# Kernel optimization log

Measured on AMD Instinct MI355X. Metric: run time of the kernel, lower is better.

## Reference

```python
import jax, jax.numpy as jnp
import numpy as np

N, E, C = 100000, 50000, 256
M, D, F, T = 128, 128, 128, 64
MSG = 2 * D + F + T  # 448
T_MAX = 100000


def setup_inputs() -> dict:
    key = jax.random.key(0)
    ks = jax.random.split(key, 16)
    src = jax.random.randint(ks[0], (E,), 0, N, dtype=jnp.int32)
    dst = jax.random.randint(ks[1], (E,), 0, N, dtype=jnp.int32)
    t = jnp.sort(jax.random.randint(ks[2], (E,), 0, T_MAX, dtype=jnp.int32))
    last_update = jax.random.randint(ks[3], (N,), 0, 1000, dtype=jnp.int32)
    event_feat = jax.random.normal(ks[4], (E, F), dtype=jnp.float32)
    src_embeds = jax.random.normal(ks[5], (E, D), dtype=jnp.float32)
    dst_embeds = jax.random.normal(ks[6], (E, D), dtype=jnp.float32)
    nodes_memory = jax.random.normal(ks[7], (N, M), dtype=jnp.float32)
    incidence = jax.random.uniform(ks[8], (N, C), dtype=jnp.float32)
    w_time = jax.random.normal(ks[9], (T,), dtype=jnp.float32)
    b_time = jax.random.normal(ks[10], (T,), dtype=jnp.float32)
    W_ih = jax.random.normal(ks[11], (MSG, 3 * M), dtype=jnp.float32) * 0.05
    W_hh = jax.random.normal(ks[12], (M, 3 * M), dtype=jnp.float32) * 0.05
    b_ih = jnp.zeros((3 * M,), jnp.float32)
    b_hh = jnp.zeros((3 * M,), jnp.float32)
    return dict(src=src, dst=dst, t=t, last_update=last_update,
                event_feat=event_feat, src_embeds=src_embeds, dst_embeds=dst_embeds,
                nodes_memory=nodes_memory, incidence=incidence,
                w_time=w_time, b_time=b_time, W_ih=W_ih, W_hh=W_hh,
                b_ih=b_ih, b_hh=b_hh)


def reference(src, dst, t, last_update, event_feat, src_embeds, dst_embeds,
              nodes_memory, incidence, w_time, b_time, W_ih, W_hh, b_ih, b_hh):
    E2 = 2 * E
    # store_events: raw messages + flipped-direction messages, keyed by source node
    src_all = jnp.concatenate([src, dst])            # [2E]
    emb_s = jnp.concatenate([src_embeds, dst_embeds], axis=0)
    emb_d = jnp.concatenate([dst_embeds, src_embeds], axis=0)
    feat = jnp.concatenate([event_feat, event_feat], axis=0)
    t_all = jnp.concatenate([t, t])                  # [2E]
    # message function: concat(src_embed, dst_embed, event_feat, time_encoding(dt))
    dt = (t_all - last_update[src_all]).astype(jnp.float32)
    time_enc = jnp.cos(dt[:, None] * w_time[None, :] + b_time[None, :])  # [2E, T]
    msg = jnp.concatenate([emb_s, emb_d, feat, time_enc], axis=-1)       # [2E, MSG]
    # 'last' aggregation: per-node argmax over timestamps via rank-encoded segment_max
    perm = jnp.argsort(t_all)  # ascending time order
    rank = jnp.zeros((E2,), jnp.int32).at[perm].set(jnp.arange(E2, dtype=jnp.int32))
    seg_rank = jax.ops.segment_max(rank, src_all, num_segments=N)
    counts = jax.ops.segment_sum(jnp.ones((E2,), jnp.int32), src_all, num_segments=N)
    has_msg = counts > 0                              # [N]
    last_idx = perm[jnp.where(has_msg, seg_rank, 0)]  # [N] event index of last message
    agg_msg = msg[last_idx]                           # [N, MSG]
    # GRU memory updater (torch.nn.GRUCell convention)
    gx = agg_msg @ W_ih + b_ih
    gh = nodes_memory @ W_hh + b_hh
    xr, xz, xn = jnp.split(gx, 3, axis=-1)
    hr, hz, hn = jnp.split(gh, 3, axis=-1)
    r = jax.nn.sigmoid(xr + hr)
    z = jax.nn.sigmoid(xz + hz)
    n = jnp.tanh(xn + r * hn)
    h_new = (1.0 - z) * n + z * nodes_memory
    new_mem = jnp.where(has_msg[:, None], h_new, nodes_memory)  # [N, M]
    # rewire_graph: community memory = incidence.T @ nodes_memory
    comm_mem = jnp.einsum('nc,nm->cm', incidence, new_mem)      # [C, M]
    return jnp.concatenate([new_mem, comm_mem], axis=0)         # [N + C, M]
```

## Files before the change

### kernel.cpp

```cpp
#include <hip/hip_runtime.h>
#include <hip/hip_bf16.h>
#include <stdint.h>

#define N_NODES   100000
#define N_EVENTS  50000
#define N_COMM    256
#define DIM_M     128
#define K_TOT     576
#define GCOLS     512
#define INV2PI    0.15915494309189535f
#define XB_GRID   4096
#define WCONV_BLOCKS ((GCOLS * K_TOT + 255) / 256)
#define COPY_BLOCKS  512

typedef float f32x4 __attribute__((ext_vector_type(4)));
typedef short s16x8 __attribute__((ext_vector_type(8)));
typedef short s16x4 __attribute__((ext_vector_type(4)));

#define KEYS_OFF   0
#define CNT_OFF    800000
#define LIST_OFF   800008
#define WT_OFF     1200640
#define X_ROWS     100096
#define X_OFF      1790464
#define PART_M_OFF X_OFF
#define CT_NCH     512
#define CT_CPN     196
#define TMP2_OFF   (PART_M_OFF + 67108864)
#define TENC_OFF   1790464
#define PART_F_OFF 14594560

__device__ inline unsigned short f2bf(float x) {
    union { float f; unsigned u; } v; v.f = x;
    unsigned r = v.u + 0x7FFFu + ((v.u >> 16) & 1u);
    return (unsigned short)(r >> 16);
}
__device__ inline float bf2f(unsigned short u) {
    union { unsigned u; float f; } v; v.u = ((unsigned)u) << 16;
    return v.f;
}
__device__ inline float cos_rev(float rev) {
    float fr = rev - floorf(rev);
#if __has_builtin(__builtin_amdgcn_cosf)
    return __builtin_amdgcn_cosf(fr);
#else
    return cosf(fr * 6.283185307179586f);
#endif
}
__device__ inline float sigmoid_f(float x) { return 1.0f / (1.0f + __expf(-x)); }
__device__ inline float tanh_f(float x) {
    float t = __expf(2.0f * x);
    return 1.0f - 2.0f / (t + 1.0f);
}

__global__ __launch_bounds__(256) void k_agg(const int* __restrict__ src,
                                             const int* __restrict__ dst,
                                             const int* __restrict__ t,
                                             unsigned long long* __restrict__ keys) {
    int i = blockIdx.x * 256 + threadIdx.x;
    if (i >= 2 * N_EVENTS) return;
    int e = (i < N_EVENTS) ? i : i - N_EVENTS;
    int node = (i < N_EVENTS) ? src[i] : dst[e];
    unsigned long long key =
        ((unsigned long long)(unsigned)t[e] << 32) | (unsigned)(i + 1);
    atomicMax(&keys[node], key);
}

__global__ __launch_bounds__(256) void k_compact(const unsigned long long* __restrict__ keys,
                                                 unsigned int* __restrict__ cnt,
                                                 int* __restrict__ list) {
    int n = blockIdx.x * 256 + threadIdx.x;
    if (n >= N_NODES) return;
    if (keys[n] != 0ULL) {
        unsigned p = atomicAdd(cnt, 1u);
        list[p] = n;
    }
}

__global__ __launch_bounds__(256) void k_xbuild(
    const unsigned long long* __restrict__ keys,
    const unsigned int* __restrict__ cnt,
    const int* __restrict__ list,
    const int* __restrict__ t,
    const int* __restrict__ last_update,
    const float* __restrict__ event_feat,
    const float* __restrict__ src_embeds,
    const float* __restrict__ dst_embeds,
    const float* __restrict__ mem,
    const float* __restrict__ w_time,
    const float* __restrict__ b_time,
    const float* __restrict__ W_ih,
    const float* __restrict__ W_hh,
    unsigned short* __restrict__ Wt,
    unsigned short* __restrict__ X,
    float* __restrict__ out) {
    if (blockIdx.x >= XB_GRID + WCONV_BLOCKS) {
        const int b = blockIdx.x - (XB_GRID + WCONV_BLOCKS);
        for (int idx = b * 256 + threadIdx.x; idx < N_NODES * 32;
             idx += COPY_BLOCKS * 256) {
            const int n = idx >> 5;
            if (keys[n] == 0ULL)
                ((float4*)out)[idx] = ((const float4*)mem)[idx];
        }
        return;
    }
    if (blockIdx.x >= XB_GRID) {
        int idx = (blockIdx.x - XB_GRID) * 256 + threadIdx.x;
        if (idx >= GCOLS * K_TOT) return;
        int col2 = idx / K_TOT, k = idx % K_TOT;
        int mh = col2 >> 8, rem = col2 & 255;
        int g = rem >> 6, m = mh * 64 + (rem & 63);
        float v;
        if (g == 0)      v = (k < 448) ? W_ih[(size_t)k * 384 + m]
                                       : W_hh[(size_t)(k - 448) * 384 + m];
        else if (g == 1) v = (k < 448) ? W_ih[(size_t)k * 384 + 128 + m]
                                       : W_hh[(size_t)(k - 448) * 384 + 128 + m];
        else if (g == 2) v = (k < 448) ? W_ih[(size_t)k * 384 + 256 + m] : 0.0f;
        else             v = (k < 448) ? 0.0f : W_hh[(size_t)(k - 448) * 384 + 256 + m];
        Wt[idx] = f2bf(v);
        return;
    }
    const unsigned c = *cnt;
    const unsigned cpad = (c + 127u) & ~127u;
    const unsigned total = cpad * 72u;
    for (unsigned idx = blockIdx.x * 256 + threadIdx.x; idx < total;
         idx += XB_GRID * 256) {
        const unsigned row = idx / 72u;
        const int s = (int)(idx - row * 72u);
        unsigned short* xp = X + (size_t)row * K_TOT + s * 8;
        s16x8 v;
        if (row >= c) {
#pragma unroll
            for (int j = 0; j < 8; ++j) v[j] = 0;
            *(s16x8*)xp = v;
            continue;
        }
        const int node = list[row];
        const unsigned long long key = keys[node];
        const int ia = (int)(key & 0xffffffffull) - 1;
        const int e = (ia < N_EVENTS) ? ia : ia - N_EVENTS;
        if (s < 48) {
            const float* p;
            if (s < 16)
                p = ((ia < N_EVENTS) ? src_embeds : dst_embeds) + (size_t)e * 128 + s * 8;
            else if (s < 32)
                p = ((ia < N_EVENTS) ? dst_embeds : src_embeds) + (size_t)e * 128 + (s - 16) * 8;
            else
                p = event_feat + (size_t)e * 128 + (s - 32) * 8;
            float4 a = *(const float4*)p;
            float4 b = *(const float4*)(p + 4);
            v[0] = (short)f2bf(a.x); v[1] = (short)f2bf(a.y);
            v[2] = (short)f2bf(a.z); v[3] = (short)f2bf(a.w);
            v[4] = (short)f2bf(b.x); v[5] = (short)f2bf(b.y);
            v[6] = (short)f2bf(b.z); v[7] = (short)f2bf(b.w);
        } else if (s < 56) {
            const float dt = (float)(t[e] - last_update[node]);
            const int c0 = (s - 48) * 8;
#pragma unroll
            for (int j = 0; j < 8; ++j) {
                float rev = fmaf(dt, w_time[c0 + j] * INV2PI, b_time[c0 + j] * INV2PI);
                v[j] = (short)f2bf(cos_rev(rev));
            }
        } else {
            const float* p = mem + (size_t)node * 128 + (s - 56) * 8;
            float4 a = *(const float4*)p;
            float4 b = *(const float4*)(p + 4);
            v[0] = (short)f2bf(a.x); v[1] = (short)f2bf(a.y);
            v[2] = (short)f2bf(a.z); v[3] = (short)f2bf(a.w);
            v[4] = (short)f2bf(b.x); v[5] = (short)f2bf(b.y);
            v[6] = (short)f2bf(b.z); v[7] = (short)f2bf(b.w);
        }
        *(s16x8*)xp = v;
    }
}

__global__ __launch_bounds__(512, 4) void k_gemm2(
    const unsigned int* __restrict__ cnt,
    const int* __restrict__ list,
    const unsigned short* __restrict__ X,
    const unsigned short* __restrict__ Wt,
    const float* __restrict__ b_ih,
    const float* __restrict__ b_hh,
    float* __restrict__ out) {
    __shared__ unsigned short As[3][128][32];
    __shared__ unsigned short Bs[3][256][32];
    __shared__ int Ls[128];

    const unsigned c = *cnt;
    const int rb = blockIdx.x >> 1;
    const int mh = blockIdx.x & 1;
    const int base = rb * 128;
    if ((unsigned)base >= c) return;
    const int tid = threadIdx.x;
    const int w = tid >> 6, l = tid & 63;
    const int lr = l & 15, lk = l >> 4;
    const int wm = w >> 2, wn = w & 3;

    if (tid < 128)
        Ls[tid] = ((unsigned)(base + tid) < c) ? list[base + tid] : 0;

    const int mcol = mh * 64 + wn * 16 + lr;

    unsigned short hreg[16];
#pragma unroll
    for (int rt = 0; rt < 4; ++rt)
#pragma unroll
        for (int reg = 0; reg < 4; ++reg) {
            const int r = wm * 64 + rt * 16 + lk * 4 + reg;
            hreg[rt * 4 + reg] = X[(size_t)(base + r) * K_TOT + 448 + mcol];
        }

    const int srow = tid >> 2;
    const int sd = tid & 3;
    const int ssl = (sd ^ ((srow >> 1) & 3)) << 3;
    const unsigned short* gA  = X  + (size_t)(base + srow) * K_TOT + ssl;
    const unsigned short* gB0 = Wt + (size_t)(mh * 256 + srow) * K_TOT + ssl;
    const unsigned short* gB1 = Wt + (size_t)(mh * 256 + 128 + srow) * K_TOT + ssl;

#define GLD(SRC, DST) __builtin_amdgcn_global_load_lds( \
        (const __attribute__((address_space(1))) unsigned int*)(SRC), \
        (__attribute__((address_space(3))) unsigned int*)(DST), 16, 0, 0)

    auto stage = [&](int ch, int buf) {
        GLD(gA  + ch * 32, &As[buf][w * 16][0]);
        GLD(gB0 + ch * 32, &Bs[buf][w * 16][0]);
        GLD(gB1 + ch * 32, &Bs[buf][128 + w * 16][0]);
    };

    f32x4 acc[4][4];
#pragma unroll
    for (int rt = 0; rt < 4; ++rt)
#pragma unroll
        for (int i = 0; i < 4; ++i) acc[rt][i] = (f32x4){0.f, 0.f, 0.f, 0.f};

    stage(0, 0);
    stage(1, 1);
    __syncthreads();

#pragma unroll
    for (int ch = 0; ch < 18; ++ch) {
        const int buf = ch % 3;
        if (ch <= 15) stage(ch + 2, (ch + 2) % 3);
        __builtin_amdgcn_s_setprio(1);
        s16x8 a[4];
#pragma unroll
        for (int rt = 0; rt < 4; ++rt) {
            const int r = wm * 64 + rt * 16 + lr;
            const int sl = lk ^ ((r >> 1) & 3);
            a[rt] = *(const s16x8*)&As[buf][r][sl << 3];
        }
#pragma unroll
        for (int i = 0; i < 4; ++i) {
            const int cl = i * 64 + wn * 16 + lr;
            const int slb = lk ^ ((cl >> 1) & 3);
            s16x8 b = *(const s16x8*)&Bs[buf][cl][slb << 3];
#pragma unroll
            for (int rt = 0; rt < 4; ++rt)
                acc[rt][i] = __builtin_amdgcn_mfma_f32_16x16x32_bf16(
                    a[rt], b, acc[rt][i], 0, 0, 0);
        }
        __builtin_amdgcn_s_setprio(0);
        if (ch < 17) {
            __builtin_amdgcn_sched_barrier(0);
            if (ch < 16) asm volatile("s_waitcnt vmcnt(3)" ::: "memory");
            else         asm volatile("s_waitcnt vmcnt(0)" ::: "memory");
            __builtin_amdgcn_s_barrier();
            __builtin_amdgcn_sched_barrier(0);
        }
    }

    const float b_r  = b_ih[mcol] + b_hh[mcol];
    const float b_z  = b_ih[128 + mcol] + b_hh[128 + mcol];
    const float b_xn = b_ih[256 + mcol];
    const float b_hn = b_hh[256 + mcol];
#pragma unroll
    for (int rt = 0; rt < 4; ++rt) {
#pragma unroll
        for (int reg = 0; reg < 4; ++reg) {
            const int r = wm * 64 + rt * 16 + lk * 4 + reg;
            const int grow = base + r;
            if ((unsigned)grow < c) {
                const int node = Ls[r];
                const float h = bf2f(hreg[rt * 4 + reg]);
                float rr = sigmoid_f(acc[rt][0][reg] + b_r);
                float zz = sigmoid_f(acc[rt][1][reg] + b_z);
                float nn = tanh_f(acc[rt][2][reg] + b_xn + rr * (acc[rt][3][reg] + b_hn));
                out[(size_t)node * 128 + mcol] = (1.0f - zz) * nn + zz * h;
            }
        }
    }
#undef GLD
}

__global__ __launch_bounds__(256) void k_copy(const unsigned long long* __restrict__ keys,
                                              const float* __restrict__ nm,
                                              float* __restrict__ out) {
    int idx = blockIdx.x * 256 + threadIdx.x;
    int n = idx >> 5;
    if (n >= N_NODES) return;
    if (keys[n] != 0ULL) return;
    ((float4*)out)[idx] = ((const float4*)nm)[idx];
}

__global__ __launch_bounds__(512) void k_comm_t(const float* __restrict__ inc,
                                                const float* __restrict__ nm,
                                                float* __restrict__ partials) {
    __shared__ unsigned short T[2][12288];

    const int bid = blockIdx.x;
    const int n0 = bid * CT_CPN;
    const int n1 = min(N_NODES, n0 + CT_CPN);
    const int ng = (n1 - n0 + 31) >> 5;
    const int tid = threadIdx.x;
    const int w = tid >> 6, l = tid & 63;
    const int lr = l & 15, lk = l >> 4;

    float vi[4][4];
    float vm[4][2];

    auto load_chunk = [&](int g) {
        const int nb = n0 + g * 32 + w * 4;
#pragma unroll
        for (int ri = 0; ri < 4; ++ri) {
            const int n = nb + ri;
            const bool ok = n < n1;
#pragma unroll
            for (int j = 0; j < 4; ++j)
                vi[ri][j] = ok ? inc[(size_t)n * N_COMM + l + 64 * j] : 0.0f;
#pragma unroll
            for (int j = 0; j < 2; ++j)
                vm[ri][j] = ok ? nm[(size_t)n * DIM_M + l + 64 * j] : 0.0f;
        }
    };
    auto write_chunk = [&](int buf) {
        unsigned short* bi = &T[buf][0];
#pragma unroll
        for (int j = 0; j < 4; ++j) {
            const int cc = l + 64 * j;
            ushort4 p = make_ushort4(f2bf(vi[0][j]), f2bf(vi[1][j]),
                                     f2bf(vi[2][j]), f2bf(vi[3][j]));
            *(ushort4*)&bi[cc * 32 + ((w ^ (cc & 7)) << 2)] = p;
        }
        unsigned short* bm = &T[buf][8192];
#pragma unroll
        for (int j = 0; j < 2; ++j) {
            const int mm = l + 64 * j;
            ushort4 p = make_ushort4(f2bf(vm[0][j]), f2bf(vm[1][j]),
                                     f2bf(vm[2][j]), f2bf(vm[3][j]));
            *(ushort4*)&bm[mm * 32 + ((w ^ (mm & 7)) << 2)] = p;
        }
    };

    f32x4 acc[2][8];
#pragma unroll
    for (int ct = 0; ct < 2; ++ct)
#pragma unroll
        for (int mt = 0; mt < 8; ++mt) acc[ct][mt] = (f32x4){0.f, 0.f, 0.f, 0.f};

    auto compute_chunk = [&](int buf) {
        const unsigned short* bi = &T[buf][0];
        const unsigned short* bm = &T[buf][8192];
        s16x8 a[2];
#pragma unroll
        for (int ct = 0; ct < 2; ++ct) {
            const int cc = (w * 2 + ct) * 16 + lr;
            s16x4 lo = *(const s16x4*)&bi[cc * 32 + (((lk * 2) ^ (cc & 7)) << 2)];
            s16x4 hi = *(const s16x4*)&bi[cc * 32 + (((lk * 2 + 1) ^ (cc & 7)) << 2)];
            a[ct] = __builtin_shufflevector(lo, hi, 0, 1, 2, 3, 4, 5, 6, 7);
        }
#pragma unroll
        for (int mt = 0; mt < 8; ++mt) {
            const int mm = mt * 16 + lr;
            s16x4 lo = *(const s16x4*)&bm[mm * 32 + (((lk * 2) ^ (mm & 7)) << 2)];
            s16x4 hi = *(const s16x4*)&bm[mm * 32 + (((lk * 2 + 1) ^ (mm & 7)) << 2)];
            s16x8 b = __builtin_shufflevector(lo, hi, 0, 1, 2, 3, 4, 5, 6, 7);
            acc[0][mt] = __builtin_amdgcn_mfma_f32_16x16x32_bf16(a[0], b, acc[0][mt], 0, 0, 0);
            acc[1][mt] = __builtin_amdgcn_mfma_f32_16x16x32_bf16(a[1], b, acc[1][mt], 0, 0, 0);
        }
    };

    load_chunk(0);
    write_chunk(0);
    __syncthreads();
    for (int g = 0; g < ng; ++g) {
        if (g + 1 < ng) load_chunk(g + 1);
        compute_chunk(g & 1);
        if (g + 1 < ng) write_chunk((g + 1) & 1);
        __syncthreads();
    }

    float* p = partials + (size_t)bid * (N_COMM * DIM_M);
#pragma unroll
    for (int ct = 0; ct < 2; ++ct)
#pragma unroll
        for (int mt = 0; mt < 8; ++mt)
            *(f32x4*)&p[(size_t)(((ct * 8 + mt) * 512) + tid) * 4] = acc[ct][mt];
}

__global__ __launch_bounds__(256) void k_comm2a(const float* __restrict__ partials,
                                                float* __restrict__ tmp) {
    const int bid = blockIdx.x;
    const int y = bid >> 5, x = bid & 31;
    const int idx4 = x * 256 + threadIdx.x;
    float4 s = make_float4(0.f, 0.f, 0.f, 0.f);
    for (int ci = 0; ci < CT_NCH / 32; ++ci) {
        float4 v = *(const float4*)&partials[(size_t)(y * (CT_NCH / 32) + ci) * (N_COMM * DIM_M) + idx4 * 4];
        s.x += v.x; s.y += v.y; s.z += v.z; s.w += v.w;
    }
    *(float4*)&tmp[(size_t)y * (N_COMM * DIM_M) + idx4 * 4] = s;
}

__global__ __launch_bounds__(256) void k_comm2b(const float* __restrict__ tmp,
                                                float* __restrict__ out) {
    const int idx4 = blockIdx.x * 256 + threadIdx.x;
    float4 s = make_float4(0.f, 0.f, 0.f, 0.f);
    for (int y = 0; y < 32; ++y) {
        float4 v = *(const float4*)&tmp[(size_t)y * (N_COMM * DIM_M) + idx4 * 4];
        s.x += v.x; s.y += v.y; s.z += v.z; s.w += v.w;
    }
    const int q = idx4 >> 9;
    const int tid = idx4 & 511;
    const int ct = q >> 3, mt = q & 7;
    const int w = tid >> 6, l = tid & 63;
    const int lr = l & 15, lk = l >> 4;
    const int mm = mt * 16 + lr;
    const float sv[4] = {s.x, s.y, s.z, s.w};
#pragma unroll
    for (int reg = 0; reg < 4; ++reg) {
        const int cc = (w * 2 + ct) * 16 + lk * 4 + reg;
        out[(size_t)N_NODES * DIM_M + (size_t)cc * DIM_M + mm] = sv[reg];
    }
}

__global__ __launch_bounds__(256) void k_wconv_old(const float* __restrict__ W_ih,
                                                   const float* __restrict__ W_hh,
                                                   unsigned short* __restrict__ Wt) {
    int idx = blockIdx.x * 256 + threadIdx.x;
    if (idx >= GCOLS * K_TOT) return;
    int col = idx / K_TOT, k = idx % K_TOT;
    float v;
    if (col < 256) {
        v = (k < 448) ? W_ih[(size_t)k * 384 + col]
                      : W_hh[(size_t)(k - 448) * 384 + col];
    } else if (col < 384) {
        v = (k < 448) ? W_ih[(size_t)k * 384 + col] : 0.0f;
    } else {
        v = (k < 448) ? 0.0f : W_hh[(size_t)(k - 448) * 384 + (col - 128)];
    }
    Wt[idx] = f2bf(v);
}

__global__ __launch_bounds__(256) void k_tenc(const unsigned long long* __restrict__ keys,
                                              const unsigned int* __restrict__ cnt,
                                              const int* __restrict__ list,
                                              const int* __restrict__ t,
                                              const int* __restrict__ last_update,
                                              const float* __restrict__ w_time,
                                              const float* __restrict__ b_time,
                                              unsigned short* __restrict__ tenc) {
    int idx = blockIdx.x * 256 + threadIdx.x;
    int r = idx >> 3, slot = idx & 7;
    const unsigned c = *cnt;
    const unsigned cpad = (c + 63u) & ~63u;
    if ((unsigned)r >= cpad) return;
    s16x8 v;
    if ((unsigned)r < c) {
        int node = list[r];
        unsigned long long key = keys[node];
        int ia = (int)(key & 0xffffffffull) - 1;
        int e = (ia < N_EVENTS) ? ia : ia - N_EVENTS;
        float dt = (float)(t[e] - last_update[node]);
#pragma unroll
        for (int j = 0; j < 8; ++j) {
            int cix = slot * 8 + j;
            float arg = __fadd_rn(__fmul_rn(dt, w_time[cix]), b_time[cix]);
            v[j] = (short)f2bf(cosf(arg));
        }
    } else {
#pragma unroll
        for (int j = 0; j < 8; ++j) v[j] = 0;
    }
    *(s16x8*)&tenc[(size_t)r * 64 + slot * 8] = v;
}

__global__ __launch_bounds__(256, 2) void k_gemm_fused(
    const unsigned long long* __restrict__ keys,
    const unsigned int* __restrict__ cnt,
    const int* __restrict__ list,
    const float* __restrict__ event_feat,
    const float* __restrict__ src_embeds,
    const float* __restrict__ dst_embeds,
    const float* __restrict__ mem,
    const unsigned short* __restrict__ tenc,
    const unsigned short* __restrict__ Wt,
    const float* __restrict__ b_ih,
    const float* __restrict__ b_hh,
    float* __restrict__ out) {
    __shared__ unsigned short Xs[2][4][64][8];

    const unsigned c = *cnt;
    const int base = blockIdx.x * 64;
    if ((unsigned)base >= c) return;
    const int tid = threadIdx.x;

    const int srow = tid >> 2;
    const int kslot = tid & 3;
    const int sgrow = base + srow;
    const bool valid = (unsigned)sgrow < c;
    const float *p_es = nullptr, *p_ed = nullptr, *p_ef = nullptr, *p_mem = nullptr;
    const unsigned short* p_te = nullptr;
    if (valid) {
        int node = list[sgrow];
        unsigned long long key = keys[node];
        int ia = (int)(key & 0xffffffffull) - 1;
        int e = (ia < N_EVENTS) ? ia : ia - N_EVENTS;
        const float* sp = src_embeds + (size_t)e * 128;
        const float* dp = dst_embeds + (size_t)e * 128;
        p_es = (ia < N_EVENTS) ? sp : dp;
        p_ed = (ia < N_EVENTS) ? dp : sp;
        p_ef = event_feat + (size_t)e * 128;
        p_te = tenc + (size_t)sgrow * 64;
        p_mem = mem + (size_t)node * 128;
    }

    auto stage = [&](int ch) {
        const int buf = ch & 1;
        const int k0 = ch * 32 + kslot * 8;
        s16x8 v;
        if (valid) {
            if (k0 < 384) {
                const float* p = (k0 < 128) ? (p_es + k0)
                               : (k0 < 256) ? (p_ed + (k0 - 128))
                                            : (p_ef + (k0 - 256));
                float4 a = *(const float4*)p;
                float4 b = *(const float4*)(p + 4);
                v[0] = (short)f2bf(a.x); v[1] = (short)f2bf(a.y);
                v[2] = (short)f2bf(a.z); v[3] = (short)f2bf(a.w);
                v[4] = (short)f2bf(b.x); v[5] = (short)f2bf(b.y);
                v[6] = (short)f2bf(b.z); v[7] = (short)f2bf(b.w);
            } else if (k0 < 448) {
                v = *(const s16x8*)(p_te + (k0 - 384));
            } else {
                const float* p = p_mem + (k0 - 448);
                float4 a = *(const float4*)p;
                float4 b = *(const float4*)(p + 4);
                v[0] = (short)f2bf(a.x); v[1] = (short)f2bf(a.y);
                v[2] = (short)f2bf(a.z); v[3] = (short)f2bf(a.w);
                v[4] = (short)f2bf(b.x); v[5] = (short)f2bf(b.y);
                v[6] = (short)f2bf(b.z); v[7] = (short)f2bf(b.w);
            }
        } else {
#pragma unroll
            for (int j = 0; j < 8; ++j) v[j] = 0;
        }
        *(s16x8*)&Xs[buf][kslot][srow][0] = v;
    };

    const int w = tid >> 6;
    const int l = tid & 63;
    const int lr = l & 15;
    const int lk = l >> 4;

    f32x4 acc[4][8];
#pragma unroll
    for (int rt = 0; rt < 4; ++rt)
#pragma unroll
        for (int i = 0; i < 8; ++i) acc[rt][i] = (f32x4){0.f, 0.f, 0.f, 0.f};

    stage(0);
    __syncthreads();

    for (int ch = 0; ch < 18; ++ch) {
        if (ch < 17) stage(ch + 1);
        const int buf = ch & 1;
        s16x8 a[4];
#pragma unroll
        for (int rt = 0; rt < 4; ++rt)
            a[rt] = *(const s16x8*)&Xs[buf][lk][rt * 16 + lr][0];
#pragma unroll
        for (int i = 0; i < 8; ++i) {
            const int col = (w + 4 * i) * 16 + lr;
            s16x8 b = *(const s16x8*)&Wt[(size_t)col * K_TOT + ch * 32 + lk * 8];
#pragma unroll
            for (int rt = 0; rt < 4; ++rt)
                acc[rt][i] = __builtin_amdgcn_mfma_f32_16x16x32_bf16(
                    a[rt], b, acc[rt][i], 0, 0, 0);
        }
        __syncthreads();
    }

#pragma unroll
    for (int jj = 0; jj < 2; ++jj) {
        const int mcol = (w + 4 * jj) * 16 + lr;
        const float b_r  = b_ih[mcol] + b_hh[mcol];
        const float b_z  = b_ih[128 + mcol] + b_hh[128 + mcol];
        const float b_xn = b_ih[256 + mcol];
        const float b_hn = b_hh[256 + mcol];
#pragma unroll
        for (int rt = 0; rt < 4; ++rt) {
#pragma unroll
            for (int reg = 0; reg < 4; ++reg) {
                const int grow = base + rt * 16 + lk * 4 + reg;
                if ((unsigned)grow < c) {
                    const int node = list[grow];
                    const float h = mem[(size_t)node * 128 + mcol];
                    float rr = sigmoid_f(acc[rt][0 + jj][reg] + b_r);
                    float zz = sigmoid_f(acc[rt][2 + jj][reg] + b_z);
                    float nn = tanh_f(acc[rt][4 + jj][reg] + b_xn +
                                      rr * (acc[rt][6 + jj][reg] + b_hn));
                    out[(size_t)node * 128 + mcol] = (1.0f - zz) * nn + zz * h;
                }
            }
        }
    }
}

__global__ __launch_bounds__(256) void k_comm1(const float* __restrict__ inc,
                                               const float* __restrict__ nm,
                                               float* __restrict__ partials,
                                               int nch, int cpn) {
    __shared__ float inc_s[2][8][128];
    __shared__ float mem_s[2][8][128];

    const int bid = blockIdx.x;
    const int ct2 = bid / nch;
    const int ch  = bid % nch;
    const int n0 = ch * cpn;
    const int n1 = min(N_NODES, n0 + cpn);
    const int tid = threadIdx.x;

    const int srow = tid >> 5;
    const int scol = (tid & 31) * 4;

    auto stage = [&](int g, int buf) {
        const int n = n0 + g * 8 + srow;
        float4 iv = make_float4(0.f, 0.f, 0.f, 0.f);
        float4 mv = make_float4(0.f, 0.f, 0.f, 0.f);
        if (n < n1) {
            iv = *(const float4*)(inc + (size_t)n * N_COMM + ct2 * 128 + scol);
            mv = *(const float4*)(nm + (size_t)n * DIM_M + scol);
        }
        *(float4*)&inc_s[buf][srow][scol] = iv;
        *(float4*)&mem_s[buf][srow][scol] = mv;
    };

    const int c0 = (tid >> 3) * 4;
    const int mb = (tid & 7) * 4;

    float acc[4][4][4];
#pragma unroll
    for (int a = 0; a < 4; ++a)
#pragma unroll
        for (int b = 0; b < 4; ++b)
#pragma unroll
            for (int d = 0; d < 4; ++d) acc[a][b][d] = 0.0f;

    const int ngrp = (n1 - n0 + 7) >> 3;
    stage(0, 0);
    __syncthreads();

    for (int g = 0; g < ngrp; ++g) {
        if (g + 1 < ngrp) stage(g + 1, (g + 1) & 1);
        const int buf = g & 1;
#pragma unroll
        for (int i = 0; i < 8; ++i) {
            const float4 cv = *(const float4*)&inc_s[buf][i][c0];
            const float ca[4] = {cv.x, cv.y, cv.z, cv.w};
#pragma unroll
            for (int j = 0; j < 4; ++j) {
                const float4 mv = *(const float4*)&mem_s[buf][i][j * 32 + mb];
                const float ma[4] = {mv.x, mv.y, mv.z, mv.w};
#pragma unroll
                for (int ci = 0; ci < 4; ++ci)
#pragma unroll
                    for (int mi = 0; mi < 4; ++mi)
                        acc[ci][j][mi] = fmaf(ca[ci], ma[mi], acc[ci][j][mi]);
            }
        }
        __syncthreads();
    }

    float* p = partials + (size_t)bid * (128 * 128);
#pragma unroll
    for (int ci = 0; ci < 4; ++ci)
#pragma unroll
        for (int j = 0; j < 4; ++j)
            *(float4*)(p + (size_t)(c0 + ci) * 128 + j * 32 + mb) =
                make_float4(acc[ci][j][0], acc[ci][j][1], acc[ci][j][2], acc[ci][j][3]);
}

__global__ __launch_bounds__(256) void k_comm2_f(const float* __restrict__ partials,
                                                 float* __restrict__ out,
                                                 int nch) {
    int idx = blockIdx.x * 256 + threadIdx.x;
    if (idx >= N_COMM * DIM_M) return;
    int cg = idx >> 7;
    int m = idx & 127;
    int ct2 = cg >> 7;
    int cl = cg & 127;
    float s = 0.0f;
    for (int ch = 0; ch < nch; ++ch)
        s += partials[((size_t)ct2 * nch + ch) * 16384 + (size_t)cl * 128 + m];
    out[(size_t)N_NODES * DIM_M + idx] = s;
}

extern "C" void kernel_launch(void* const* d_in, const int* in_sizes, int n_in,
                              void* d_out, int out_size, void* d_ws, size_t ws_size,
                              hipStream_t stream) {
    const int* src          = (const int*)d_in[0];
    const int* dst          = (const int*)d_in[1];
    const int* t            = (const int*)d_in[2];
    const int* last_update  = (const int*)d_in[3];
    const float* event_feat = (const float*)d_in[4];
    const float* src_embeds = (const float*)d_in[5];
    const float* dst_embeds = (const float*)d_in[6];
    const float* nodes_mem  = (const float*)d_in[7];
    const float* incidence  = (const float*)d_in[8];
    const float* w_time     = (const float*)d_in[9];
    const float* b_time     = (const float*)d_in[10];
    const float* W_ih       = (const float*)d_in[11];
    const float* W_hh       = (const float*)d_in[12];
    const float* b_ih       = (const float*)d_in[13];
    const float* b_hh       = (const float*)d_in[14];
    float* out = (float*)d_out;

    char* ws = (char*)d_ws;
    unsigned long long* keys = (unsigned long long*)(ws + KEYS_OFF);
    unsigned int* cnt        = (unsigned int*)(ws + CNT_OFF);
    int* list                = (int*)(ws + LIST_OFF);
    unsigned short* Wt       = (unsigned short*)(ws + WT_OFF);

    const bool xfit = ws_size >= (size_t)X_OFF + (size_t)X_ROWS * (K_TOT * 2);

    hipMemsetAsync(d_ws, 0, LIST_OFF, stream);

    k_agg<<<(2 * N_EVENTS + 255) / 256, 256, 0, stream>>>(src, dst, t, keys);
    k_compact<<<(N_NODES + 255) / 256, 256, 0, stream>>>(keys, cnt, list);

    if (xfit) {
        unsigned short* X = (unsigned short*)(ws + X_OFF);
        float* partials   = (float*)(ws + PART_M_OFF);
        float* tmp2       = (float*)(ws + TMP2_OFF);

        k_xbuild<<<XB_GRID + WCONV_BLOCKS + COPY_BLOCKS, 256, 0, stream>>>(
            keys, cnt, list, t, last_update, event_feat, src_embeds, dst_embeds,
            nodes_mem, w_time, b_time, W_ih, W_hh, Wt, X, out);
        k_gemm2<<<(X_ROWS / 128) * 2, 512, 0, stream>>>(cnt, list, X, Wt,
                                                        b_ih, b_hh, out);
        k_comm_t<<<CT_NCH, 512, 0, stream>>>(incidence, out, partials);
        k_comm2a<<<1024, 256, 0, stream>>>(partials, tmp2);
        k_comm2b<<<32, 256, 0, stream>>>(tmp2, out);
    } else {
        unsigned short* tenc = (unsigned short*)(ws + TENC_OFF);
        float* partials      = (float*)(ws + PART_F_OFF);
        int NCH = 512;
        while (NCH > 8 && (size_t)PART_F_OFF + (size_t)NCH * 131072 > ws_size) NCH >>= 1;
        int cpn = (N_NODES + NCH - 1) / NCH;

        k_wconv_old<<<(GCOLS * K_TOT + 255) / 256, 256, 0, stream>>>(W_ih, W_hh, Wt);
        k_tenc<<<(100032 * 8) / 256, 256, 0, stream>>>(keys, cnt, list, t, last_update,
                                                       w_time, b_time, tenc);
        k_gemm_fused<<<100032 / 64, 256, 0, stream>>>(keys, cnt, list, event_feat,
                                                      src_embeds, dst_embeds, nodes_mem,
                                                      tenc, Wt, b_ih, b_hh, out);
        k_copy<<<(N_NODES * 32 + 255) / 256, 256, 0, stream>>>(keys, nodes_mem, out);
        k_comm1<<<2 * NCH, 256, 0, stream>>>(incidence, out, partials, NCH, cpn);
        k_comm2_f<<<(N_COMM * DIM_M + 255) / 256, 256, 0, stream>>>(partials, out, NCH);
    }
}
```

Measured before the change: 218.9 us.

## Precompute per-row event info in compact and load GEMM B operand directly to registers

The compaction kernel now records node, event index and time delta per compacted row, so the message-building kernel reads one int4 instead of chasing list, keys, t and last_update. In the GEMM, the weight (B) tiles are no longer staged through LDS; each lane loads its bf16 fragment straight from global memory into registers with a one-step prefetch, while only A stays in the triple-buffered LDS pipeline. This cuts LDS traffic and footprint but relies on the cache to serve repeated weight reads from every block, and it increases register pressure.

Result: slower. 252.4 us, median of 2 (+15.3%).

```diff
diff --git a/kernel.cpp b/kernel.cpp
--- a/kernel.cpp
+++ b/kernel.cpp
@@ -20,13 +20,15 @@
 #define KEYS_OFF   0
 #define CNT_OFF    800000
 #define LIST_OFF   800008
-#define WT_OFF     1200640
+#define EINFO_OFF  1200064
+#define WT_OFF     2800128
 #define X_ROWS     100096
-#define X_OFF      1790464
+#define X_OFF      3390208
 #define PART_M_OFF X_OFF
 #define CT_NCH     512
 #define CT_CPN     196
 #define TMP2_OFF   (PART_M_OFF + 67108864)
+#define WT_F_OFF   1200640
 #define TENC_OFF   1790464
 #define PART_F_OFF 14594560
 
@@ -67,22 +69,28 @@
 }
 
 __global__ __launch_bounds__(256) void k_compact(const unsigned long long* __restrict__ keys,
+                                                 const int* __restrict__ t,
+                                                 const int* __restrict__ last_update,
                                                  unsigned int* __restrict__ cnt,
-                                                 int* __restrict__ list) {
+                                                 int* __restrict__ list,
+                                                 int4* __restrict__ einfo) {
     int n = blockIdx.x * 256 + threadIdx.x;
     if (n >= N_NODES) return;
-    if (keys[n] != 0ULL) {
+    const unsigned long long key = keys[n];
+    if (key != 0ULL) {
         unsigned p = atomicAdd(cnt, 1u);
         list[p] = n;
+        const int ia = (int)(key & 0xffffffffull) - 1;
+        const int e = (ia < N_EVENTS) ? ia : ia - N_EVENTS;
+        const float dt = (float)(t[e] - last_update[n]);
+        einfo[p] = make_int4(n, ia, __float_as_int(dt), 0);
     }
 }
 
 __global__ __launch_bounds__(256) void k_xbuild(
     const unsigned long long* __restrict__ keys,
     const unsigned int* __restrict__ cnt,
-    const int* __restrict__ list,
-    const int* __restrict__ t,
-    const int* __restrict__ last_update,
+    const int4* __restrict__ einfo,
     const float* __restrict__ event_feat,
     const float* __restrict__ src_embeds,
     const float* __restrict__ dst_embeds,
@@ -135,9 +143,9 @@
             *(s16x8*)xp = v;
             continue;
         }
-        const int node = list[row];
-        const unsigned long long key = keys[node];
-        const int ia = (int)(key & 0xffffffffull) - 1;
+        const int4 ei = einfo[row];
+        const int node = ei.x;
+        const int ia = ei.y;
         const int e = (ia < N_EVENTS) ? ia : ia - N_EVENTS;
         if (s < 48) {
             const float* p;
@@ -154,7 +162,7 @@
             v[4] = (short)f2bf(b.x); v[5] = (short)f2bf(b.y);
             v[6] = (short)f2bf(b.z); v[7] = (short)f2bf(b.w);
         } else if (s < 56) {
-            const float dt = (float)(t[e] - last_update[node]);
+            const float dt = __int_as_float(ei.z);
             const int c0 = (s - 48) * 8;
 #pragma unroll
             for (int j = 0; j < 8; ++j) {
@@ -183,7 +191,6 @@
     const float* __restrict__ b_hh,
     float* __restrict__ out) {
     __shared__ unsigned short As[3][128][32];
-    __shared__ unsigned short Bs[3][256][32];
     __shared__ int Ls[128];
 
     const unsigned c = *cnt;
@@ -213,59 +220,70 @@
     const int srow = tid >> 2;
     const int sd = tid & 3;
     const int ssl = (sd ^ ((srow >> 1) & 3)) << 3;
-    const unsigned short* gA  = X  + (size_t)(base + srow) * K_TOT + ssl;
-    const unsigned short* gB0 = Wt + (size_t)(mh * 256 + srow) * K_TOT + ssl;
-    const unsigned short* gB1 = Wt + (size_t)(mh * 256 + 128 + srow) * K_TOT + ssl;
+    const unsigned short* gA = X + (size_t)(base + srow) * K_TOT + ssl;
+
+    const unsigned short* bp[4];
+#pragma unroll
+    for (int i = 0; i < 4; ++i)
+        bp[i] = Wt + (size_t)(mh * 256 + i * 64 + wn * 16 + lr) * K_TOT + lk * 8;
 
 #define GLD(SRC, DST) __builtin_amdgcn_global_load_lds( \
         (const __attribute__((address_space(1))) unsigned int*)(SRC), \
         (__attribute__((address_space(3))) unsigned int*)(DST), 16, 0, 0)
 
-    auto stage = [&](int ch, int buf) {
-        GLD(gA  + ch * 32, &As[buf][w * 16][0]);
-        GLD(gB0 + ch * 32, &Bs[buf][w * 16][0]);
-        GLD(gB1 + ch * 32, &Bs[buf][128 + w * 16][0]);
-    };
-
     f32x4 acc[4][4];
 #pragma unroll
     for (int rt = 0; rt < 4; ++rt)
 #pragma unroll
         for (int i = 0; i < 4; ++i) acc[rt][i] = (f32x4){0.f, 0.f, 0.f, 0.f};
 
-    stage(0, 0);
-    stage(1, 1);
+    s16x8 bcur[4], bnext[4];
+#pragma unroll
+    for (int i = 0; i < 4; ++i) bcur[i] = *(const s16x8*)(bp[i]);
+    GLD(gA, &As[0][srow][0]);
+    GLD(gA + 32, &As[1][srow][0]);
     __syncthreads();
 
 #pragma unroll
     for (int ch = 0; ch < 18; ++ch) {
-        const int buf = ch % 3;
-        if (ch <= 15) stage(ch + 2, (ch + 2) % 3);
+        if (ch < 17) {
+#pragma unroll
+            for (int i = 0; i < 4; ++i)
+                bnext[i] = *(const s16x8*)(bp[i] + (ch + 1) * 32);
+        }
+        if (ch <= 15) GLD(gA + (ch + 2) * 32, &As[(ch + 2) % 3][srow][0]);
+        __builtin_amdgcn_sched_barrier(0);
         __builtin_amdgcn_s_setprio(1);
-        s16x8 a[4];
-#pragma unroll
-        for (int rt = 0; rt < 4; ++rt) {
-            const int r = wm * 64 + rt * 16 + lr;
-            const int sl = lk ^ ((r >> 1) & 3);
-            a[rt] = *(const s16x8*)&As[buf][r][sl << 3];
-        }
-#pragma unroll
-        for (int i = 0; i < 4; ++i) {
-            const int cl = i * 64 + wn * 16 + lr;
-            const int slb = lk ^ ((cl >> 1) & 3);
-            s16x8 b = *(const s16x8*)&Bs[buf][cl][slb << 3];
-#pragma unroll
-            for (int rt = 0; rt < 4; ++rt)
-                acc[rt][i] = __builtin_amdgcn_mfma_f32_16x16x32_bf16(
-                    a[rt], b, acc[rt][i], 0, 0, 0);
+        {
+            const int buf = ch % 3;
+            s16x8 a[4];
+#pragma unroll
+            for (int rt = 0; rt < 4; ++rt) {
+                const int r = wm * 64 + rt * 16 + lr;
+                const int sl = lk ^ ((r >> 1) & 3);
+                a[rt] = *(const s16x8*)&As[buf][r][sl << 3];
+            }
+#pragma unroll
+            for (int i = 0; i < 4; ++i)
+#pragma unroll
+                for (int rt = 0; rt < 4; ++rt)
+                    acc[rt][i] = __builtin_amdgcn_mfma_f32_16x16x32_bf16(
+                        a[rt], bcur[i], acc[rt][i], 0, 0, 0);
         }
         __builtin_amdgcn_s_setprio(0);
-        if (ch < 17) {
-            __builtin_amdgcn_sched_barrier(0);
-            if (ch < 16) asm volatile("s_waitcnt vmcnt(3)" ::: "memory");
-            else         asm volatile("s_waitcnt vmcnt(0)" ::: "memory");
+        __builtin_amdgcn_sched_barrier(0);
+        if (ch < 16) {
+            asm volatile("s_waitcnt vmcnt(1)" ::: "memory");
             __builtin_amdgcn_s_barrier();
             __builtin_amdgcn_sched_barrier(0);
+        } else if (ch == 16) {
+            asm volatile("s_waitcnt vmcnt(0)" ::: "memory");
+            __builtin_amdgcn_s_barrier();
+            __builtin_amdgcn_sched_barrier(0);
+        }
+        if (ch < 17) {
+#pragma unroll
+            for (int i = 0; i < 4; ++i) bcur[i] = bnext[i];
         }
     }
 
@@ -728,22 +746,24 @@
     unsigned long long* keys = (unsigned long long*)(ws + KEYS_OFF);
     unsigned int* cnt        = (unsigned int*)(ws + CNT_OFF);
     int* list                = (int*)(ws + LIST_OFF);
-    unsigned short* Wt       = (unsigned short*)(ws + WT_OFF);
+    int4* einfo              = (int4*)(ws + EINFO_OFF);
 
     const bool xfit = ws_size >= (size_t)X_OFF + (size_t)X_ROWS * (K_TOT * 2);
 
     hipMemsetAsync(d_ws, 0, LIST_OFF, stream);
 
     k_agg<<<(2 * N_EVENTS + 255) / 256, 256, 0, stream>>>(src, dst, t, keys);
-    k_compact<<<(N_NODES + 255) / 256, 256, 0, stream>>>(keys, cnt, list);
+    k_compact<<<(N_NODES + 255) / 256, 256, 0, stream>>>(keys, t, last_update,
+                                                         cnt, list, einfo);
 
     if (xfit) {
-        unsigned short* X = (unsigned short*)(ws + X_OFF);
-        float* partials   = (float*)(ws + PART_M_OFF);
-        float* tmp2       = (float*)(ws + TMP2_OFF);
+        unsigned short* Wt = (unsigned short*)(ws + WT_OFF);
+        unsigned short* X  = (unsigned short*)(ws + X_OFF);
+        float* partials    = (float*)(ws + PART_M_OFF);
+        float* tmp2        = (float*)(ws + TMP2_OFF);
 
         k_xbuild<<<XB_GRID + WCONV_BLOCKS + COPY_BLOCKS, 256, 0, stream>>>(
-            keys, cnt, list, t, last_update, event_feat, src_embeds, dst_embeds,
+            keys, cnt, einfo, event_feat, src_embeds, dst_embeds,
             nodes_mem, w_time, b_time, W_ih, W_hh, Wt, X, out);
         k_gemm2<<<(X_ROWS / 128) * 2, 512, 0, stream>>>(cnt, list, X, Wt,
                                                         b_ih, b_hh, out);
@@ -751,6 +771,7 @@
         k_comm2a<<<1024, 256, 0, stream>>>(partials, tmp2);
         k_comm2b<<<32, 256, 0, stream>>>(tmp2, out);
     } else {
+        unsigned short* Wt   = (unsigned short*)(ws + WT_F_OFF);
         unsigned short* tenc = (unsigned short*)(ws + TENC_OFF);
         float* partials      = (float*)(ws + PART_F_OFF);
         int NCH = 512;
```
